# Kernel tuning notes

Measured on AMD Instinct MI355X. Metric: run time of the kernel, lower is better.

The kernel has to match this reference:

```python
import jax, jax.numpy as jnp
import numpy as np

H, E, N, R = 1024, 2048, 16, 64  # hidden, expand, state, dt_rank
B, L = 2, 2048


def setup_inputs() -> dict:
    key = jax.random.key(0)
    ks = jax.random.split(key, 20)
    s = 0.02
    inp = {
        "x": jax.random.normal(ks[0], (B, L, H), jnp.float32),
        "ln_gamma": jnp.ones((H,), jnp.float32),
        "ln_beta": jnp.zeros((H,), jnp.float32),
        "W_in": jax.random.normal(ks[1], (H, 2 * E), jnp.float32) * s,
        "b_in": jnp.zeros((2 * E,), jnp.float32),
        "W_delta": jax.random.normal(ks[2], (E, R), jnp.float32) * s,
        "b_delta": jnp.zeros((R,), jnp.float32),
        "W_dt": jax.random.normal(ks[3], (R, E), jnp.float32) * s,
        "b_dt": jnp.zeros((E,), jnp.float32),
        "W_B": jax.random.normal(ks[4], (E, N), jnp.float32) * s,
        "b_B": jnp.zeros((N,), jnp.float32),
        "W_C": jax.random.normal(ks[5], (E, N), jnp.float32) * s,
        "b_C": jnp.zeros((N,), jnp.float32),
        "A_log": -jnp.exp(jax.random.normal(ks[6], (E, N), jnp.float32) * 0.1),
        "D": jax.random.normal(ks[7], (E,), jnp.float32) * 0.1,
        "W_out": jax.random.normal(ks[8], (E, H), jnp.float32) * s,
        "b_out": jnp.zeros((H,), jnp.float32),
    }
    return inp


def _layer_norm(x, gamma, beta, eps=1e-5):
    mu = jnp.mean(x, axis=-1, keepdims=True)
    var = jnp.var(x, axis=-1, keepdims=True)
    return (x - mu) * jax.lax.rsqrt(var + eps) * gamma + beta


def _selective_scan(x, delta, A, Bm, Cm):
    # x, delta: [B,L,E]; Bm, Cm: [B,L,N]; A: [E,N]
    def step(h, inputs):
        x_t, d_t, B_t, C_t = inputs  # [B,E],[B,E],[B,N],[B,N]
        A_disc = jnp.exp(d_t[..., None] * A)                     # [B,E,N]
        h = A_disc * h + d_t[..., None] * B_t[:, None, :] * x_t[..., None]
        y_t = jnp.einsum('bn,ben->be', C_t, h)
        return h, y_t

    h0 = jnp.zeros((x.shape[0], A.shape[0], A.shape[1]), x.dtype)
    xs = (jnp.swapaxes(x, 0, 1), jnp.swapaxes(delta, 0, 1),
          jnp.swapaxes(Bm, 0, 1), jnp.swapaxes(Cm, 0, 1))
    _, ys = jax.lax.scan(step, h0, xs)  # ys: [L,B,E]
    return jnp.swapaxes(ys, 0, 1)


def reference(x, ln_gamma, ln_beta, W_in, b_in, W_delta, b_delta, W_dt, b_dt,
              W_B, b_B, W_C, b_C, A_log, D, W_out, b_out):
    residual = x
    xn = _layer_norm(x, ln_gamma, ln_beta)
    x_proj = xn @ W_in + b_in                     # [B,L,2E]
    u, gate = jnp.split(x_proj, 2, axis=-1)
    u = jax.nn.silu(u)
    delta = jax.nn.softplus((u @ W_delta + b_delta) @ W_dt + b_dt)  # [B,L,E]
    Bm = u @ W_B + b_B                            # [B,L,N]
    Cm = u @ W_C + b_C                            # [B,L,N]
    A = -jnp.exp(A_log)                           # [E,N]
    y = _selective_scan(u, delta, A, Bm, Cm)
    y = y + u * D
    y = y * jax.nn.silu(gate)
    return y @ W_out + b_out + residual
```

## Files before the change

### kernel.cpp

```cpp
#include <hip/hip_runtime.h>
#include <stdint.h>

#define DH 1024
#define DE 2048
#define DN 16
#define DR 64
#define DB 2
#define DL 2048
#define DT (DB * DL)

typedef short short8 __attribute__((ext_vector_type(8)));
typedef float f32x4 __attribute__((ext_vector_type(4)));

__device__ __forceinline__ float bf2f(uint32_t u) {
  union { uint32_t i; float f; } v; v.i = u << 16; return v.f;
}
__device__ __forceinline__ unsigned short f2bf(float f) {
  union { float f; uint32_t i; } v; v.f = f;
  uint32_t r = v.i + 0x7FFFu + ((v.i >> 16) & 1u);
  return (unsigned short)(r >> 16);
}
__device__ __forceinline__ float ldsc(const void* p, size_t i, bool f32) {
  return f32 ? ((const float*)p)[i] : bf2f(((const unsigned short*)p)[i]);
}
__device__ __forceinline__ float4 ld4(const void* p, size_t i, bool f32) {
  if (f32) return *(const float4*)((const float*)p + i);
  ushort4 v = *(const ushort4*)((const unsigned short*)p + i);
  return make_float4(bf2f(v.x), bf2f(v.y), bf2f(v.z), bf2f(v.w));
}

__device__ __forceinline__ void gll16(const unsigned short* g, unsigned short* l) {
  __builtin_amdgcn_global_load_lds(
      (const __attribute__((address_space(1))) unsigned int*)g,
      (__attribute__((address_space(3))) unsigned int*)l, 16, 0, 0);
}

__device__ __forceinline__ void transpose_tile(
    const void* src, unsigned short* dst, int K, int N, int bx, int by,
    int tid, bool f32, float (*tile)[33]) {
  const int tx = tid & 31;
  const int ty = tid >> 5;
  const int kb = by * 32, nb = bx * 32;
  #pragma unroll
  for (int i = 0; i < 4; ++i)
    tile[ty + 8 * i][tx] = ldsc(src, (size_t)(kb + ty + 8 * i) * N + nb + tx, f32);
  __syncthreads();
  #pragma unroll
  for (int i = 0; i < 4; ++i)
    dst[(size_t)(nb + ty + 8 * i) * K + kb + tx] = f2bf(tile[tx][ty + 8 * i]);
}

__global__ __launch_bounds__(256) void k_convert_all(
    const void* __restrict__ W_in, const void* __restrict__ W_out,
    const void* __restrict__ W_dt, const void* __restrict__ Wd,
    const void* __restrict__ Wb, const void* __restrict__ Wc,
    const void* __restrict__ b_in, const void* __restrict__ b_out,
    const void* __restrict__ b_delta, const void* __restrict__ b_B,
    const void* __restrict__ b_C, const void* __restrict__ A_log,
    const void* __restrict__ Dvec, const void* __restrict__ b_dt,
    unsigned short* __restrict__ WtIn, unsigned short* __restrict__ WtOut,
    unsigned short* __restrict__ WtDt, unsigned short* __restrict__ WtDbc,
    float* __restrict__ bin, float* __restrict__ bout,
    float* __restrict__ bdbc, float* __restrict__ Ac, float* __restrict__ Dv,
    float* __restrict__ bdt,
    const uint32_t* __restrict__ probe) {
  const bool f32 = (probe[0] == 0x3F800000u);
  __shared__ float tile[32][33];
  const int tid = threadIdx.x;
  int f = blockIdx.x;
  if (f < 4096) {
    transpose_tile(W_in, WtIn, 1024, 4096, f & 127, f >> 7, tid, f32, tile);
    return;
  }
  f -= 4096;
  if (f < 2048) {
    transpose_tile(W_out, WtOut, 2048, 1024, f & 31, f >> 5, tid, f32, tile);
    return;
  }
  f -= 2048;
  if (f < 128) {
    transpose_tile(W_dt, WtDt, 64, 2048, f & 63, f >> 6, tid, f32, tile);
    return;
  }
  f -= 128;
  if (f < 1024) {
    const int idx = f * 256 + tid;
    const int c = idx >> 11, k = idx & 2047;
    float v = 0.f;
    if (c < 64) v = ldsc(Wd, (size_t)k * DR + c, f32);
    else if (c < 80) v = ldsc(Wb, (size_t)k * DN + (c - 64), f32);
    else if (c < 96) v = ldsc(Wc, (size_t)k * DN + (c - 80), f32);
    WtDbc[idx] = f2bf(v);
    return;
  }
  f -= 1024;
  {
    int i = f * 256 + tid;
    if (i < 4096) { bin[i] = ldsc(b_in, i, f32); return; }
    i -= 4096;
    if (i < 1024) { bout[i] = ldsc(b_out, i, f32); return; }
    i -= 1024;
    if (i < 128) {
      float v = 0.f;
      if (i < 64) v = ldsc(b_delta, i, f32);
      else if (i < 80) v = ldsc(b_B, i - 64, f32);
      else if (i < 96) v = ldsc(b_C, i - 80, f32);
      bdbc[i] = v; return;
    }
    i -= 128;
    if (i < 32768) { Ac[i] = -__expf(ldsc(A_log, i, f32)); return; }
    i -= 32768;
    if (i < 2048) { Dv[i] = ldsc(Dvec, i, f32); return; }
    i -= 2048;
    if (i < 2048) { bdt[i] = ldsc(b_dt, i, f32); }
  }
}

__global__ __launch_bounds__(256) void k_dbc_reduce(
    const float* __restrict__ Part, const float* __restrict__ bdbc,
    unsigned short* __restrict__ dt1b, float* __restrict__ dtBC, int MT) {
  const int gid = blockIdx.x * 256 + threadIdx.x;
  const int row = gid / 96, col = gid - row * 96;
  if (row >= MT) return;
  float s = bdbc[col];
  const size_t stride = (size_t)MT * 96;
  #pragma unroll
  for (int kp = 0; kp < 8; ++kp)
    s += Part[(size_t)kp * stride + (size_t)row * 96 + col];
  if (col < 64) dt1b[(size_t)row * 64 + col] = f2bf(s);
  else dtBC[(size_t)row * 32 + (col - 64)] = s;
}

__global__ __launch_bounds__(256) void k_out_reduce(
    const float* __restrict__ Part2, const float* __restrict__ bout,
    const void* __restrict__ resid, void* __restrict__ dout,
    int MT, int t0, int lgTc, const uint32_t* __restrict__ probe) {
  const bool f32 = (probe[0] == 0x3F800000u);
  const int gid = blockIdx.x * 256 + threadIdx.x;
  const int base = gid * 4;
  const int row = base >> 10;
  const int col = base & 1023;
  if (row >= MT) return;
  const int tcm = (1 << lgTc) - 1;
  const size_t grow = (size_t)((row >> lgTc) * DL + t0 + (row & tcm));
  const size_t ms = (size_t)MT * 1024;
  float4 p0 = *(const float4*)(Part2 + (size_t)row * 1024 + col);
  float4 p1 = *(const float4*)(Part2 + ms + (size_t)row * 1024 + col);
  float4 bo = *(const float4*)(bout + col);
  float4 rs = ld4(resid, grow * 1024 + col, f32);
  float4 o;
  o.x = p0.x + p1.x + bo.x + rs.x;
  o.y = p0.y + p1.y + bo.y + rs.y;
  o.z = p0.z + p1.z + bo.z + rs.z;
  o.w = p0.w + p1.w + bo.w + rs.w;
  if (f32) {
    *(float4*)((float*)dout + grow * 1024 + col) = o;
  } else {
    ushort4 u;
    u.x = f2bf(o.x); u.y = f2bf(o.y); u.z = f2bf(o.z); u.w = f2bf(o.w);
    *(ushort4*)((unsigned short*)dout + grow * 1024 + col) = u;
  }
}

__global__ __launch_bounds__(256) void ln_bf16(
    const void* __restrict__ x, const void* __restrict__ gamma,
    const void* __restrict__ beta, unsigned short* __restrict__ xn,
    int t0, int lgTc, const uint32_t* __restrict__ probe) {
  const bool f32 = (probe[0] == 0x3F800000u);
  const int row = blockIdx.x;
  const int tid = threadIdx.x;
  const int tcm = (1 << lgTc) - 1;
  const int grow = (row >> lgTc) * DL + t0 + (row & tcm);
  float4 v = ld4(x, (size_t)grow * DH + tid * 4, f32);
  float s = v.x + v.y + v.z + v.w;
  float ss = v.x * v.x + v.y * v.y + v.z * v.z + v.w * v.w;
  #pragma unroll
  for (int off = 32; off > 0; off >>= 1) {
    s += __shfl_down(s, off, 64);
    ss += __shfl_down(ss, off, 64);
  }
  __shared__ float sbuf[4], ssbuf[4];
  const int wave = tid >> 6, lane = tid & 63;
  if (lane == 0) { sbuf[wave] = s; ssbuf[wave] = ss; }
  __syncthreads();
  float tot = sbuf[0] + sbuf[1] + sbuf[2] + sbuf[3];
  float tots = ssbuf[0] + ssbuf[1] + ssbuf[2] + ssbuf[3];
  const float inv = 1.0f / (float)DH;
  float mu = tot * inv;
  float var = tots * inv - mu * mu;
  float rs = rsqrtf(var + 1e-5f);
  float4 gv = ld4(gamma, tid * 4, f32);
  float4 bv = ld4(beta, tid * 4, f32);
  ushort4 o;
  o.x = f2bf((v.x - mu) * rs * gv.x + bv.x);
  o.y = f2bf((v.y - mu) * rs * gv.y + bv.y);
  o.z = f2bf((v.z - mu) * rs * gv.z + bv.z);
  o.w = f2bf((v.w - mu) * rs * gv.w + bv.w);
  *(ushort4*)(xn + (size_t)row * DH + tid * 4) = o;
}

__global__ __launch_bounds__(256) void gemm_mfma(
    const unsigned short* __restrict__ A, int lda,
    const unsigned short* __restrict__ Wt,
    const float* __restrict__ bias,
    const void* __restrict__ resid,
    void* __restrict__ C, int ldc,
    int K, int mode, int t0, int lgTc,
    const uint32_t* __restrict__ probe) {
  __shared__ unsigned short As[2][4096];
  __shared__ unsigned short Bs[2][4096];
  const int tid = threadIdx.x;
  const int wid = tid >> 6;
  const int lane = tid & 63;
  const int quad = lane >> 4;
  const int l16 = lane & 15;
  const int wm = (wid & 1) * 64;
  const int wn = (wid >> 1) * 64;
  const int m0 = blockIdx.y * 128;
  int n0 = blockIdx.x * 128;
  int kbeg = 0, kend = K;
  if (mode == 5) {
    const int Ks = K >> 3; kbeg = blockIdx.x * Ks; kend = kbeg + Ks; n0 = 0;
  } else if (mode == 6) {
    const int Ks = K >> 1; const int kp = blockIdx.x >> 3;
    kbeg = kp * Ks; kend = kbeg + Ks; n0 = (blockIdx.x & 7) * 128;
  }
  const int sr = tid >> 2;
  const int sc = (tid & 3) * 8;

  const unsigned short* gA0 = A + (size_t)(m0 + sr) * lda + sc;
  const unsigned short* gA1 = A + (size_t)(m0 + sr + 64) * lda + sc;
  const unsigned short* gB0 = Wt + (size_t)(n0 + sr) * K + sc;
  const unsigned short* gB1 = Wt + (size_t)(n0 + sr + 64) * K + sc;
  const int wb = (tid & 192) * 8;
  unsigned short* lA00 = &As[0][wb];
  unsigned short* lA01 = &As[1][wb];
  unsigned short* lA10 = &As[0][2048 + wb];
  unsigned short* lA11 = &As[1][2048 + wb];
  unsigned short* lB00 = &Bs[0][wb];
  unsigned short* lB01 = &Bs[1][wb];
  unsigned short* lB10 = &Bs[0][2048 + wb];
  unsigned short* lB11 = &Bs[1][2048 + wb];

  f32x4 acc[4][4];
  #pragma unroll
  for (int i = 0; i < 4; ++i)
    #pragma unroll
    for (int j = 0; j < 4; ++j) {
      acc[i][j][0] = 0.f; acc[i][j][1] = 0.f;
      acc[i][j][2] = 0.f; acc[i][j][3] = 0.f;
    }

  for (int k0 = kbeg; k0 < kend; k0 += 64) {
    gll16(gA0 + k0, lA00);
    gll16(gA0 + k0 + 32, lA01);
    gll16(gA1 + k0, lA10);
    gll16(gA1 + k0 + 32, lA11);
    gll16(gB0 + k0, lB00);
    gll16(gB0 + k0 + 32, lB01);
    gll16(gB1 + k0, lB10);
    gll16(gB1 + k0 + 32, lB11);
    __syncthreads();
    #pragma unroll
    for (int ks = 0; ks < 2; ++ks) {
      short8 af[4], bf[4];
      #pragma unroll
      for (int i = 0; i < 4; ++i)
        af[i] = *(const short8*)(&As[ks][(wm + i * 16 + l16) * 32 + quad * 8]);
      #pragma unroll
      for (int j = 0; j < 4; ++j)
        bf[j] = *(const short8*)(&Bs[ks][(wn + j * 16 + l16) * 32 + quad * 8]);
      #pragma unroll
      for (int i = 0; i < 4; ++i)
        #pragma unroll
        for (int j = 0; j < 4; ++j)
          acc[i][j] = __builtin_amdgcn_mfma_f32_16x16x32_bf16(af[i], bf[j], acc[i][j], 0, 0, 0);
    }
    __syncthreads();
  }

  const int tcm = (1 << lgTc) - 1;
  const bool f32 = (probe[0] == 0x3F800000u);
  #pragma unroll
  for (int i = 0; i < 4; ++i) {
    #pragma unroll
    for (int j = 0; j < 4; ++j) {
      const int col = n0 + wn + j * 16 + l16;
      const float bsv = (mode == 5 || mode == 6) ? 0.f : bias[col];
      #pragma unroll
      for (int r = 0; r < 4; ++r) {
        const int row = m0 + wm + i * 16 + quad * 4 + r;
        float v = acc[i][j][r] + bsv;
        if (mode == 1) {
          if (col < DE) v = v / (1.f + __expf(-v));
          ((unsigned short*)C)[(size_t)row * ldc + col] = f2bf(v);
        } else if (mode == 2) {
          v = (v > 15.0f) ? v : log1pf(__expf(v));
          ((unsigned short*)C)[(size_t)row * ldc + col] = f2bf(v);
        } else if (mode == 5) {
          if (col < 96) {
            const size_t kpb = (size_t)blockIdx.x * ((size_t)gridDim.y * 128) * 96;
            ((float*)C)[kpb + (size_t)row * 96 + col] = v;
          }
        } else if (mode == 6) {
          const size_t kpb = (size_t)(blockIdx.x >> 3) * ((size_t)gridDim.y * 128) * 1024;
          ((float*)C)[kpb + (size_t)row * 1024 + col] = v;
        } else {
          const size_t grow = (size_t)((row >> lgTc) * DL + t0 + (row & tcm));
          v += ldsc(resid, grow * ldc + col, f32);
          if (f32) ((float*)C)[grow * ldc + col] = v;
          else ((unsigned short*)C)[grow * ldc + col] = f2bf(v);
        }
      }
    }
  }
}

__global__ __launch_bounds__(256) void scan_phaseA(
    const unsigned short* __restrict__ xproj,
    const unsigned short* __restrict__ delta,
    const float* __restrict__ dtBC,
    const float* __restrict__ Ac,
    float* __restrict__ Aprod,
    float* __restrict__ Hpart,
    int Tc, int P) {
  const int tid = threadIdx.x;
  const int ng = tid & 3;
  const int e = blockIdx.x * 64 + (tid >> 2);
  const int bs = blockIdx.y;
  const int S = Tc / P;
  const int b = bs / S, s = bs - b * S;
  const int r0 = b * Tc + s * P;

  const float4 ac = *(const float4*)(Ac + (size_t)e * 16 + ng * 4);
  const unsigned short* dp = delta + (size_t)r0 * 2048 + e;
  const unsigned short* xp = xproj + (size_t)r0 * 4096 + e;
  const float* bp = dtBC + (size_t)r0 * 32 + ng * 4;

  float4 ap = make_float4(1.f, 1.f, 1.f, 1.f);
  float4 h = make_float4(0.f, 0.f, 0.f, 0.f);
  for (int t = 0; t < P; ++t) {
    const float d = bf2f(*dp);
    const float x = bf2f(*xp);
    const float4 B = *(const float4*)bp;
    const float a0 = __expf(d * ac.x), a1 = __expf(d * ac.y),
                a2 = __expf(d * ac.z), a3 = __expf(d * ac.w);
    ap.x *= a0; ap.y *= a1; ap.z *= a2; ap.w *= a3;
    const float dx = d * x;
    h.x = a0 * h.x + dx * B.x;
    h.y = a1 * h.y + dx * B.y;
    h.z = a2 * h.z + dx * B.z;
    h.w = a3 * h.w + dx * B.w;
    dp += 2048; xp += 4096; bp += 32;
  }
  const size_t o = ((size_t)bs * 2048 + e) * 16 + ng * 4;
  *(float4*)(Aprod + o) = ap;
  *(float4*)(Hpart + o) = h;
}

__global__ __launch_bounds__(256) void scan_phaseB(
    const float* __restrict__ Aprod, const float* __restrict__ Hpart,
    float* __restrict__ Hstart,
    float* __restrict__ hstate,
    int S, int first) {
  const int gid = blockIdx.x * 256 + threadIdx.x;
  const int b = gid >> 13;
  const int en4 = gid & 8191;
  float4 h = first ? make_float4(0.f, 0.f, 0.f, 0.f)
                   : ((const float4*)hstate)[gid];
  for (int s = 0; s < S; ++s) {
    const size_t o = ((size_t)(b * S + s) << 13) + en4;
    ((float4*)Hstart)[o] = h;
    const float4 a = ((const float4*)Aprod)[o];
    const float4 p = ((const float4*)Hpart)[o];
    h.x = a.x * h.x + p.x;
    h.y = a.y * h.y + p.y;
    h.z = a.z * h.z + p.z;
    h.w = a.w * h.w + p.w;
  }
  ((float4*)hstate)[gid] = h;
}

__global__ __launch_bounds__(256) void scan_phaseC(
    unsigned short* __restrict__ xproj,
    const unsigned short* __restrict__ delta,
    const float* __restrict__ dtBC,
    const float* __restrict__ Ac,
    const float* __restrict__ Dv,
    const float* __restrict__ Hstart,
    int Tc, int P) {
  const int tid = threadIdx.x;
  const int ng = tid & 3;
  const int e = blockIdx.x * 64 + (tid >> 2);
  const int bs = blockIdx.y;
  const int S = Tc / P;
  const int b = bs / S, s = bs - b * S;
  const int r0 = b * Tc + s * P;

  const float4 ac = *(const float4*)(Ac + (size_t)e * 16 + ng * 4);
  const float dv = Dv[e];
  float4 h = *(const float4*)(Hstart + ((size_t)bs * 2048 + e) * 16 + ng * 4);

  const unsigned short* dp = delta + (size_t)r0 * 2048 + e;
  unsigned short* xp = xproj + (size_t)r0 * 4096 + e;
  const float* bp = dtBC + (size_t)r0 * 32 + ng * 4;

  for (int t = 0; t < P; ++t) {
    const float d = bf2f(*dp);
    const float x = bf2f(xp[0]);
    const float4 B = *(const float4*)bp;
    const float4 Cc = *(const float4*)(bp + 16);
    const float a0 = __expf(d * ac.x), a1 = __expf(d * ac.y),
                a2 = __expf(d * ac.z), a3 = __expf(d * ac.w);
    const float dx = d * x;
    h.x = a0 * h.x + dx * B.x;
    h.y = a1 * h.y + dx * B.y;
    h.z = a2 * h.z + dx * B.z;
    h.w = a3 * h.w + dx * B.w;
    float y = h.x * Cc.x + h.y * Cc.y + h.z * Cc.z + h.w * Cc.w;
    y += __shfl_xor(y, 1, 64);
    y += __shfl_xor(y, 2, 64);
    const float g = bf2f(xp[2048]);
    const float sg = g / (1.f + __expf(-g));
    const unsigned short outv = f2bf((y + x * dv) * sg);
    if (ng == 0) xp[2048] = outv;
    dp += 2048; xp += 4096; bp += 32;
  }
}

__global__ __launch_bounds__(256) void ln_kernel(
    const void* __restrict__ x, const void* __restrict__ gamma,
    const void* __restrict__ beta, float* __restrict__ xn,
    int t0, int lgTc, const uint32_t* __restrict__ probe) {
  const bool f32 = (probe[0] == 0x3F800000u);
  const int row = blockIdx.x;
  const int tid = threadIdx.x;
  const int tcm = (1 << lgTc) - 1;
  const int grow = (row >> lgTc) * DL + t0 + (row & tcm);
  float4 v = ld4(x, (size_t)grow * DH + tid * 4, f32);
  float s = v.x + v.y + v.z + v.w;
  float ss = v.x * v.x + v.y * v.y + v.z * v.z + v.w * v.w;
  #pragma unroll
  for (int off = 32; off > 0; off >>= 1) {
    s += __shfl_down(s, off, 64);
    ss += __shfl_down(ss, off, 64);
  }
  __shared__ float sbuf[4], ssbuf[4];
  const int wave = tid >> 6, lane = tid & 63;
  if (lane == 0) { sbuf[wave] = s; ssbuf[wave] = ss; }
  __syncthreads();
  float tot = sbuf[0] + sbuf[1] + sbuf[2] + sbuf[3];
  float tots = ssbuf[0] + ssbuf[1] + ssbuf[2] + ssbuf[3];
  const float inv = 1.0f / (float)DH;
  float mu = tot * inv;
  float var = tots * inv - mu * mu;
  float rs = rsqrtf(var + 1e-5f);
  float4 gv = ld4(gamma, tid * 4, f32);
  float4 bv = ld4(beta, tid * 4, f32);
  float4 o;
  o.x = (v.x - mu) * rs * gv.x + bv.x;
  o.y = (v.y - mu) * rs * gv.y + bv.y;
  o.z = (v.z - mu) * rs * gv.z + bv.z;
  o.w = (v.w - mu) * rs * gv.w + bv.w;
  *(float4*)(xn + (size_t)row * DH + tid * 4) = o;
}

#define BM 64
#define BN 64
#define BK 16
__global__ __launch_bounds__(256) void gemm_k(
    const float* __restrict__ A, int lda,
    const void* __restrict__ W,
    const void* __restrict__ bias,
    const void* __restrict__ resid,
    void* __restrict__ C, int ldc, int c_output,
    int N, int K, int mode, int t0, int lgTc,
    const uint32_t* __restrict__ probe) {
  const bool f32 = (probe[0] == 0x3F800000u);
  __shared__ float As[BM][BK + 1];
  __shared__ float Bs[BK][BN + 4];
  const int tid = threadIdx.x;
  const int tx = tid & 15;
  const int ty = tid >> 4;
  const int m0 = blockIdx.y * BM;
  const int n0 = blockIdx.x * BN;
  const int aRow = tid >> 2;
  const int aCol = (tid & 3) << 2;
  const int bRow = tid >> 4;
  const int bCol = (tid & 15) << 2;

  float acc[4][4];
  #pragma unroll
  for (int i = 0; i < 4; ++i)
    #pragma unroll
    for (int j = 0; j < 4; ++j) acc[i][j] = 0.f;

  for (int k0 = 0; k0 < K; k0 += BK) {
    float4 av = *(const float4*)(A + (size_t)(m0 + aRow) * lda + (k0 + aCol));
    As[aRow][aCol + 0] = av.x;
    As[aRow][aCol + 1] = av.y;
    As[aRow][aCol + 2] = av.z;
    As[aRow][aCol + 3] = av.w;
    if (n0 + bCol < N) {
      float4 bv = ld4(W, (size_t)(k0 + bRow) * N + (n0 + bCol), f32);
      Bs[bRow][bCol + 0] = bv.x;
      Bs[bRow][bCol + 1] = bv.y;
      Bs[bRow][bCol + 2] = bv.z;
      Bs[bRow][bCol + 3] = bv.w;
    } else {
      Bs[bRow][bCol + 0] = 0.f;
      Bs[bRow][bCol + 1] = 0.f;
      Bs[bRow][bCol + 2] = 0.f;
      Bs[bRow][bCol + 3] = 0.f;
    }
    __syncthreads();
    #pragma unroll
    for (int k = 0; k < BK; ++k) {
      float a0 = As[ty * 4 + 0][k];
      float a1 = As[ty * 4 + 1][k];
      float a2 = As[ty * 4 + 2][k];
      float a3 = As[ty * 4 + 3][k];
      float b0 = Bs[k][tx * 4 + 0];
      float b1 = Bs[k][tx * 4 + 1];
      float b2 = Bs[k][tx * 4 + 2];
      float b3 = Bs[k][tx * 4 + 3];
      acc[0][0] += a0 * b0; acc[0][1] += a0 * b1; acc[0][2] += a0 * b2; acc[0][3] += a0 * b3;
      acc[1][0] += a1 * b0; acc[1][1] += a1 * b1; acc[1][2] += a1 * b2; acc[1][3] += a1 * b3;
      acc[2][0] += a2 * b0; acc[2][1] += a2 * b1; acc[2][2] += a2 * b2; acc[2][3] += a2 * b3;
      acc[3][0] += a3 * b0; acc[3][1] += a3 * b1; acc[3][2] += a3 * b2; acc[3][3] += a3 * b3;
    }
    __syncthreads();
  }

  const int tcm = (1 << lgTc) - 1;
  #pragma unroll
  for (int i = 0; i < 4; ++i) {
    const int gm = m0 + ty * 4 + i;
    #pragma unroll
    for (int j = 0; j < 4; ++j) {
      const int gn = n0 + tx * 4 + j;
      if (gn < N) {
        float v = acc[i][j] + ldsc(bias, gn, f32);
        size_t crow = (size_t)gm;
        if (mode == 1) {
          if (gn < DE) v = v / (1.0f + __expf(-v));
        } else if (mode == 2) {
          v = (v > 15.0f) ? v : log1pf(__expf(v));
        } else if (mode == 3) {
          const size_t grow = (size_t)((gm >> lgTc) * DL + t0 + (gm & tcm));
          v += ldsc(resid, grow * ldc + gn, f32);
          crow = grow;
        }
        if (c_output) {
          if (f32) ((float*)C)[crow * ldc + gn] = v;
          else ((unsigned short*)C)[crow * ldc + gn] = f2bf(v);
        } else {
          ((float*)C)[crow * ldc + gn] = v;
        }
      }
    }
  }
}

__global__ __launch_bounds__(256) void scan_kernel(
    float* __restrict__ xproj, const float* __restrict__ delta,
    const float* __restrict__ Bmat, const float* __restrict__ Cmat,
    const void* __restrict__ A_log, const void* __restrict__ Dvec,
    float* __restrict__ hstate, int Tc, int first,
    const uint32_t* __restrict__ probe) {
  const bool f32 = (probe[0] == 0x3F800000u);
  const int gid = blockIdx.x * 256 + threadIdx.x;
  const int b = gid >> 11;
  const int e = gid & (DE - 1);
  float Ac[DN];
  #pragma unroll
  for (int n = 0; n < DN; ++n) Ac[n] = -__expf(ldsc(A_log, (size_t)e * DN + n, f32));
  const float Dvl = ldsc(Dvec, e, f32);
  float h[DN];
  float* hs = hstate + ((size_t)b * DE + e) * DN;
  if (first) {
    #pragma unroll
    for (int n = 0; n < DN; ++n) h[n] = 0.f;
  } else {
    #pragma unroll
    for (int n = 0; n < DN; ++n) h[n] = hs[n];
  }
  for (int t = 0; t < Tc; ++t) {
    const size_t r = (size_t)(b * Tc + t);
    const float x = xproj[r * (2 * DE) + e];
    const float g = xproj[r * (2 * DE) + DE + e];
    const float d = delta[r * DE + e];
    const float4* bp = (const float4*)(Bmat + r * DN);
    const float4* cp = (const float4*)(Cmat + r * DN);
    float4 b0 = bp[0], b1 = bp[1], b2 = bp[2], b3 = bp[3];
    float4 c0 = cp[0], c1 = cp[1], c2 = cp[2], c3 = cp[3];
    float Bv[DN] = {b0.x,b0.y,b0.z,b0.w, b1.x,b1.y,b1.z,b1.w,
                    b2.x,b2.y,b2.z,b2.w, b3.x,b3.y,b3.z,b3.w};
    float Cv[DN] = {c0.x,c0.y,c0.z,c0.w, c1.x,c1.y,c1.z,c1.w,
                    c2.x,c2.y,c2.z,c2.w, c3.x,c3.y,c3.z,c3.w};
    const float dx = d * x;
    float y = 0.f;
    #pragma unroll
    for (int n = 0; n < DN; ++n) {
      float ad = __expf(d * Ac[n]);
      h[n] = ad * h[n] + dx * Bv[n];
      y += Cv[n] * h[n];
    }
    const float sg = g / (1.0f + __expf(-g));
    xproj[r * (2 * DE) + DE + e] = (y + x * Dvl) * sg;
  }
  #pragma unroll
  for (int n = 0; n < DN; ++n) hs[n] = h[n];
}

extern "C" void kernel_launch(void* const* d_in, const int* in_sizes, int n_in,
                              void* d_out, int out_size, void* d_ws, size_t ws_size,
                              hipStream_t stream) {
  const void* x = d_in[0];
  const void* ln_gamma = d_in[1];
  const void* ln_beta = d_in[2];
  const void* W_in = d_in[3];
  const void* b_in = d_in[4];
  const void* W_delta = d_in[5];
  const void* b_delta = d_in[6];
  const void* W_dt = d_in[7];
  const void* b_dt = d_in[8];
  const void* W_B = d_in[9];
  const void* b_B = d_in[10];
  const void* W_C = d_in[11];
  const void* b_C = d_in[12];
  const void* A_log = d_in[13];
  const void* Dvec = d_in[14];
  const void* W_out = d_in[15];
  const void* b_out = d_in[16];
  const uint32_t* probe = (const uint32_t*)ln_gamma;
  char* ws = (char*)d_ws;

  const size_t P_WTIN = (size_t)4096 * 1024 * 2;
  const size_t P_WTOUT = (size_t)1024 * 2048 * 2;
  const size_t P_WDBC = (size_t)128 * 2048 * 2;
  const size_t P_WDT = (size_t)2048 * 64 * 2;
  const size_t P_F32 = (size_t)(4096 + 1024 + 128 + 32768 + 2048 + 2048 + 65536) * 4;
  const size_t persist = P_WTIN + P_WTOUT + P_WDBC + P_WDT + P_F32;
  auto chunk_bytes = [](int Tc) {
    const int P = Tc < 64 ? Tc : 64;
    const size_t S = (size_t)(Tc / P);
    const size_t MT = (size_t)DB * Tc;
    size_t tail = MT * (2048 * 2 + 8 * 96 * 4) + 3 * (size_t)DB * S * 32768 * 4;
    size_t part2 = MT * 8192;
    if (part2 > tail) tail = part2;
    return MT * ((1024 + 4096 + 64) * 2 + 32 * 4) + tail;
  };
  int lgTc = -1;
  for (int lg = 11; lg >= 6; --lg) {
    if (persist + chunk_bytes(1 << lg) + 4096 <= ws_size) { lgTc = lg; break; }
  }

  if (lgTc >= 0) {
    const int Tc = 1 << lgTc;
    const int MT = DB * Tc;
    const int nchunks = DL / Tc;
    const int P = Tc < 64 ? Tc : 64;
    const int S = Tc / P;

    size_t off = 0;
    unsigned short* WtIn = (unsigned short*)(ws + off); off += P_WTIN;
    unsigned short* WtOut = (unsigned short*)(ws + off); off += P_WTOUT;
    unsigned short* WtDbc = (unsigned short*)(ws + off); off += P_WDBC;
    unsigned short* WtDt = (unsigned short*)(ws + off); off += P_WDT;
    float* bin = (float*)(ws + off); off += 4096 * 4;
    float* bout = (float*)(ws + off); off += 1024 * 4;
    float* bdbc = (float*)(ws + off); off += 128 * 4;
    float* bdt = (float*)(ws + off); off += 2048 * 4;
    float* Ac = (float*)(ws + off); off += 32768 * 4;
    float* Dv = (float*)(ws + off); off += 2048 * 4;
    float* hstate = (float*)(ws + off); off += 65536 * 4;
    unsigned short* xn = (unsigned short*)(ws + off); off += (size_t)MT * 1024 * 2;
    unsigned short* xproj = (unsigned short*)(ws + off); off += (size_t)MT * 4096 * 2;
    unsigned short* dt1b = (unsigned short*)(ws + off); off += (size_t)MT * 64 * 2;
    float* dtBC = (float*)(ws + off); off += (size_t)MT * 32 * 4;
    char* alias0 = ws + off;
    unsigned short* delta = (unsigned short*)(alias0);
    float* Part = (float*)(alias0 + (size_t)MT * 2048 * 2);
    float* Aprod = (float*)(alias0 + (size_t)MT * 2048 * 2 + (size_t)8 * MT * 96 * 4);
    float* Hpart = Aprod + (size_t)DB * S * 32768;
    float* Hstart = Hpart + (size_t)DB * S * 32768;
    float* Part2 = (float*)(alias0);

    k_convert_all<<<7469, 256, 0, stream>>>(
        W_in, W_out, W_dt, W_delta, W_B, W_C,
        b_in, b_out, b_delta, b_B, b_C, A_log, Dvec, b_dt,
        WtIn, WtOut, WtDt, WtDbc, bin, bout, bdbc, Ac, Dv, bdt, probe);

    for (int c = 0; c < nchunks; ++c) {
      const int t0 = c * Tc;
      ln_bf16<<<MT, 256, 0, stream>>>(x, ln_gamma, ln_beta, xn, t0, lgTc, probe);
      gemm_mfma<<<dim3(4096 / 128, MT / 128), 256, 0, stream>>>(
          xn, 1024, WtIn, bin, nullptr, xproj, 4096, 1024, 1, 0, 0, probe);
      gemm_mfma<<<dim3(8, MT / 128), 256, 0, stream>>>(
          xproj, 4096, WtDbc, bdbc, nullptr, Part, 96, 2048, 5, 0, 0, probe);
      k_dbc_reduce<<<(MT * 96 + 255) / 256, 256, 0, stream>>>(
          Part, bdbc, dt1b, dtBC, MT);
      gemm_mfma<<<dim3(2048 / 128, MT / 128), 256, 0, stream>>>(
          dt1b, 64, WtDt, bdt, nullptr, delta, 2048, 64, 2, 0, 0, probe);
      scan_phaseA<<<dim3(32, DB * S), 256, 0, stream>>>(
          xproj, delta, dtBC, Ac, Aprod, Hpart, Tc, P);
      scan_phaseB<<<64, 256, 0, stream>>>(
          Aprod, Hpart, Hstart, hstate, S, c == 0 ? 1 : 0);
      scan_phaseC<<<dim3(32, DB * S), 256, 0, stream>>>(
          xproj, delta, dtBC, Ac, Dv, Hstart, Tc, P);
      gemm_mfma<<<dim3(16, MT / 128), 256, 0, stream>>>(
          xproj + DE, 4096, WtOut, bout, nullptr, Part2, 1024, 2048, 6, 0, 0, probe);
      k_out_reduce<<<MT, 256, 0, stream>>>(
          Part2, bout, x, d_out, MT, t0, lgTc, probe);
    }
    return;
  }

  {
    int lg = 8;
    while (lg > 6 &&
           ((size_t)(2u << lg) * 7264 * 4 + (size_t)DB * DE * DN * 4 + 4096) > ws_size)
      --lg;
    const int Tc = 1 << lg;
    const int MT = DB * Tc;
    const int nchunks = DL / Tc;

    size_t off = 0;
    float* xproj_c = (float*)(ws + off); off += (size_t)MT * 2 * DE * 4;
    float* xn_c    = (float*)(ws + off); off += (size_t)MT * DH * 4;
    float* delta_c = (float*)(ws + off); off += (size_t)MT * DE * 4;
    float* dt1_c   = (float*)(ws + off); off += (size_t)MT * DR * 4;
    float* Bm_c    = (float*)(ws + off); off += (size_t)MT * DN * 4;
    float* Cm_c    = (float*)(ws + off); off += (size_t)MT * DN * 4;
    float* hstate  = (float*)(ws + off);

    for (int c = 0; c < nchunks; ++c) {
      const int t0 = c * Tc;
      ln_kernel<<<MT, 256, 0, stream>>>(x, ln_gamma, ln_beta, xn_c, t0, lg, probe);
      gemm_k<<<dim3(2 * DE / BN, MT / BM), 256, 0, stream>>>(
          xn_c, DH, W_in, b_in, nullptr, xproj_c, 2 * DE, 0, 2 * DE, DH, 1, 0, 0, probe);
      gemm_k<<<dim3(1, MT / BM), 256, 0, stream>>>(
          xproj_c, 2 * DE, W_delta, b_delta, nullptr, dt1_c, DR, 0, DR, DE, 0, 0, 0, probe);
      gemm_k<<<dim3(DE / BN, MT / BM), 256, 0, stream>>>(
          dt1_c, DR, W_dt, b_dt, nullptr, delta_c, DE, 0, DE, DR, 2, 0, 0, probe);
      gemm_k<<<dim3(1, MT / BM), 256, 0, stream>>>(
          xproj_c, 2 * DE, W_B, b_B, nullptr, Bm_c, DN, 0, DN, DE, 0, 0, 0, probe);
      gemm_k<<<dim3(1, MT / BM), 256, 0, stream>>>(
          xproj_c, 2 * DE, W_C, b_C, nullptr, Cm_c, DN, 0, DN, DE, 0, 0, 0, probe);
      scan_kernel<<<16, 256, 0, stream>>>(
          xproj_c, delta_c, Bm_c, Cm_c, A_log, Dvec, hstate, Tc, c == 0 ? 1 : 0, probe);
      gemm_k<<<dim3(DH / BN, MT / BM), 256, 0, stream>>>(
          xproj_c + DE, 2 * DE, W_out, b_out, x, d_out, DH, 1, DH, DE, 3, t0, lg, probe);
    }
  }
}
```

Baseline: 445.4 us.

## Load GEMM MFMA fragments directly from global memory instead of LDS staging

```diff
diff --git a/kernel.cpp b/kernel.cpp
--- a/kernel.cpp
+++ b/kernel.cpp
@@ -27,12 +27,6 @@
   if (f32) return *(const float4*)((const float*)p + i);
   ushort4 v = *(const ushort4*)((const unsigned short*)p + i);
   return make_float4(bf2f(v.x), bf2f(v.y), bf2f(v.z), bf2f(v.w));
-}
-
-__device__ __forceinline__ void gll16(const unsigned short* g, unsigned short* l) {
-  __builtin_amdgcn_global_load_lds(
-      (const __attribute__((address_space(1))) unsigned int*)g,
-      (__attribute__((address_space(3))) unsigned int*)l, 16, 0, 0);
 }
 
 __device__ __forceinline__ void transpose_tile(
@@ -207,8 +201,6 @@
     void* __restrict__ C, int ldc,
     int K, int mode, int t0, int lgTc,
     const uint32_t* __restrict__ probe) {
-  __shared__ unsigned short As[2][4096];
-  __shared__ unsigned short Bs[2][4096];
   const int tid = threadIdx.x;
   const int wid = tid >> 6;
   const int lane = tid & 63;
@@ -225,22 +217,15 @@
     const int Ks = K >> 1; const int kp = blockIdx.x >> 3;
     kbeg = kp * Ks; kend = kbeg + Ks; n0 = (blockIdx.x & 7) * 128;
   }
-  const int sr = tid >> 2;
-  const int sc = (tid & 3) * 8;
-
-  const unsigned short* gA0 = A + (size_t)(m0 + sr) * lda + sc;
-  const unsigned short* gA1 = A + (size_t)(m0 + sr + 64) * lda + sc;
-  const unsigned short* gB0 = Wt + (size_t)(n0 + sr) * K + sc;
-  const unsigned short* gB1 = Wt + (size_t)(n0 + sr + 64) * K + sc;
-  const int wb = (tid & 192) * 8;
-  unsigned short* lA00 = &As[0][wb];
-  unsigned short* lA01 = &As[1][wb];
-  unsigned short* lA10 = &As[0][2048 + wb];
-  unsigned short* lA11 = &As[1][2048 + wb];
-  unsigned short* lB00 = &Bs[0][wb];
-  unsigned short* lB01 = &Bs[1][wb];
-  unsigned short* lB10 = &Bs[0][2048 + wb];
-  unsigned short* lB11 = &Bs[1][2048 + wb];
+
+  const unsigned short* pa[4];
+  const unsigned short* pb[4];
+  #pragma unroll
+  for (int i = 0; i < 4; ++i)
+    pa[i] = A + (size_t)(m0 + wm + i * 16 + l16) * lda + kbeg + quad * 8;
+  #pragma unroll
+  for (int j = 0; j < 4; ++j)
+    pb[j] = Wt + (size_t)(n0 + wn + j * 16 + l16) * K + kbeg + quad * 8;
 
   f32x4 acc[4][4];
   #pragma unroll
@@ -251,32 +236,22 @@
       acc[i][j][2] = 0.f; acc[i][j][3] = 0.f;
     }
 
-  for (int k0 = kbeg; k0 < kend; k0 += 64) {
-    gll16(gA0 + k0, lA00);
-    gll16(gA0 + k0 + 32, lA01);
-    gll16(gA1 + k0, lA10);
-    gll16(gA1 + k0 + 32, lA11);
-    gll16(gB0 + k0, lB00);
-    gll16(gB0 + k0 + 32, lB01);
-    gll16(gB1 + k0, lB10);
-    gll16(gB1 + k0 + 32, lB11);
-    __syncthreads();
-    #pragma unroll
-    for (int ks = 0; ks < 2; ++ks) {
-      short8 af[4], bf[4];
-      #pragma unroll
-      for (int i = 0; i < 4; ++i)
-        af[i] = *(const short8*)(&As[ks][(wm + i * 16 + l16) * 32 + quad * 8]);
+  const int nsteps = (kend - kbeg) >> 5;
+  for (int s = 0; s < nsteps; ++s) {
+    short8 af[4], bf[4];
+    #pragma unroll
+    for (int i = 0; i < 4; ++i) af[i] = *(const short8*)pa[i];
+    #pragma unroll
+    for (int j = 0; j < 4; ++j) bf[j] = *(const short8*)pb[j];
+    #pragma unroll
+    for (int i = 0; i < 4; ++i) pa[i] += 32;
+    #pragma unroll
+    for (int j = 0; j < 4; ++j) pb[j] += 32;
+    #pragma unroll
+    for (int i = 0; i < 4; ++i)
       #pragma unroll
       for (int j = 0; j < 4; ++j)
-        bf[j] = *(const short8*)(&Bs[ks][(wn + j * 16 + l16) * 32 + quad * 8]);
-      #pragma unroll
-      for (int i = 0; i < 4; ++i)
-        #pragma unroll
-        for (int j = 0; j < 4; ++j)
-          acc[i][j] = __builtin_amdgcn_mfma_f32_16x16x32_bf16(af[i], bf[j], acc[i][j], 0, 0, 0);
-    }
-    __syncthreads();
+        acc[i][j] = __builtin_amdgcn_mfma_f32_16x16x32_bf16(af[i], bf[j], acc[i][j], 0, 0, 0);
   }
 
   const int tcm = (1 << lgTc) - 1;
```

Result: slower. 547.0 us (+22.8%).
